# Optimization experiments

Measured on AMD Instinct MI355X. Metric: run time of the kernel, lower is better.

## Reference

```python
import jax, jax.numpy as jnp
import numpy as np

ALPHA = 3.0
TOP_K = 16
N_NODES = 8192
EMB_DIM = 128


def setup_inputs() -> dict:
    key = jax.random.key(0)
    k1, k2, k3, k4, k5, k6 = jax.random.split(key, 6)
    return {
        "idx": jnp.arange(N_NODES, dtype=jnp.int64 if jax.config.jax_enable_x64 else jnp.int32),
        "emb1_w": jax.random.normal(k1, (N_NODES, EMB_DIM), dtype=jnp.float32),
        "emb2_w": jax.random.normal(k2, (N_NODES, EMB_DIM), dtype=jnp.float32),
        "th1_w": jax.random.normal(k3, (EMB_DIM, EMB_DIM), dtype=jnp.float32) * 0.08,
        "th1_b": jax.random.normal(k4, (EMB_DIM,), dtype=jnp.float32) * 0.02,
        "th2_w": jax.random.normal(k5, (EMB_DIM, EMB_DIM), dtype=jnp.float32) * 0.08,
        "th2_b": jax.random.normal(k6, (EMB_DIM,), dtype=jnp.float32) * 0.02,
    }


def reference(idx, emb1_w, emb2_w, th1_w, th1_b, th2_w, th2_b):
    # embedding lookup + linear + tanh (nn.Linear: x @ W.T + b)
    e1 = jnp.tanh(ALPHA * (emb1_w[idx] @ th1_w.T + th1_b))  # [N, D]
    e2 = jnp.tanh(ALPHA * (emb2_w[idx] @ th2_w.T + th2_b))  # [N, D]
    # antisymmetric score -> tanh -> relu  => [N, N]
    adj = jax.nn.relu(jnp.tanh(ALPHA * (e1 @ e2.T - e2 @ e1.T)))
    # eval-mode top-k per row, scatter a binary mask (s1.fill_(1) in the source)
    _, t1 = jax.lax.top_k(adj, TOP_K)  # [N, k]
    n = idx.shape[0]
    rows = jnp.arange(n)[:, None]
    mask = jnp.zeros((n, n), dtype=adj.dtype).at[rows, t1].set(1.0)
    return adj * mask
```

## Files before the change

kernel.cpp:

```cpp
#include <hip/hip_runtime.h>

#define NN    8192
#define DD    128
#define TOPK  16

#define CUT_D 7.99881172180175781
#define CUT_F 7.99881172180175781f
#define EPS_F 2.0e-2f


__global__ __launch_bounds__(256) void k1ws(
    const int* __restrict__ idx,
    const float* __restrict__ emb1, const float* __restrict__ W1, const float* __restrict__ b1,
    const float* __restrict__ emb2, const float* __restrict__ W2, const float* __restrict__ b2,
    float* __restrict__ e1ws, float* __restrict__ e2ws)
{
    const float* emb; const float* W; const float* bias; float* eo;
    if (blockIdx.y == 0) { emb = emb1; W = W1; bias = b1; eo = e1ws; }
    else                 { emb = emb2; W = W2; bias = b2; eo = e2ws; }

    __shared__ float Wl[128][65];
    __shared__ float Xl[16][65];
    __shared__ int rowi[16];

    int t  = threadIdx.x;
    int r0 = blockIdx.x * 16;
    if (t < 16) {
        bool wide = (idx[1] == 0 && idx[2] == 1);
        int row = wide ? idx[2 * (r0 + t)] : idx[r0 + t];
        rowi[t] = min(max(row, 0), NN - 1);
    }
    __syncthreads();

    int d = t & 127, rh = t >> 7;
    double acc[8];
    #pragma unroll
    for (int q = 0; q < 8; q++) acc[q] = 0.0;

    for (int h = 0; h < 2; h++) {
        if (h) __syncthreads();
        for (int i = t; i < 128 * 64; i += 256)
            Wl[i >> 6][i & 63] = W[(i >> 6) * DD + h * 64 + (i & 63)];
        for (int i = t; i < 16 * 64; i += 256)
            Xl[i >> 6][i & 63] = emb[(size_t)rowi[i >> 6] * DD + h * 64 + (i & 63)];
        __syncthreads();
        for (int k = 0; k < 64; k++) {
            double wv = (double)Wl[d][k];
            #pragma unroll
            for (int q = 0; q < 8; q++) acc[q] += (double)Xl[rh + 2 * q][k] * wv;
        }
    }
    double bv = (double)bias[d];
    #pragma unroll
    for (int q = 0; q < 8; q++)
        eo[(size_t)(r0 + rh + 2 * q) * DD + d] = (float)tanh(3.0 * (acc[q] + bv));
}

__global__ __launch_bounds__(256) void kselfill(
    const float* __restrict__ e1, const float* __restrict__ e2,
    float* __restrict__ out)
{
    __shared__ union {
        struct { float A1[32][36], A2[32][36], B1[32][132], B2[32][132]; } p;
        float pref[32][128];
        float vals[NN];
    } sm;
    __shared__ unsigned int cls32[32][32];
    __shared__ int fb[32];
    __shared__ float redv[256];
    __shared__ int   redi[256];
    __shared__ unsigned int si[TOPK];
    __shared__ float sv[TOPK];

    int ti = blockIdx.x;
    int t  = threadIdx.x;
    int rx = t & 31, ry = t >> 5;
    int mc0 = rx * 4, mr0 = ry * 4;

    float acc[4][4];
    #pragma unroll
    for (int r = 0; r < 4; r++)
        #pragma unroll
        for (int c = 0; c < 4; c++) acc[r][c] = 0.f;

    for (int h = 0; h < 4; h++) {
        __syncthreads();
        {
            int rr = t >> 3, dq = t & 7;
            int o  = h * 32 + dq * 4;
            float4 va1 = *(const float4*)&e1[(size_t)(ti * 32 + rr) * DD + o];
            float4 va2 = *(const float4*)&e2[(size_t)(ti * 32 + rr) * DD + o];
            int dd = dq * 4;
            sm.p.A1[dd+0][rr] = va1.x; sm.p.A1[dd+1][rr] = va1.y;
            sm.p.A1[dd+2][rr] = va1.z; sm.p.A1[dd+3][rr] = va1.w;
            sm.p.A2[dd+0][rr] = va2.x; sm.p.A2[dd+1][rr] = va2.y;
            sm.p.A2[dd+2][rr] = va2.z; sm.p.A2[dd+3][rr] = va2.w;
        }
        #pragma unroll
        for (int it2 = 0; it2 < 4; it2++) {
            int id = it2 * 256 + t;
            int rr = id >> 3, dq = id & 7;
            int o  = h * 32 + dq * 4;
            float4 vb1 = *(const float4*)&e1[(size_t)rr * DD + o];
            float4 vb2 = *(const float4*)&e2[(size_t)rr * DD + o];
            int dd = dq * 4;
            sm.p.B1[dd+0][rr] = vb1.x; sm.p.B1[dd+1][rr] = vb1.y;
            sm.p.B1[dd+2][rr] = vb1.z; sm.p.B1[dd+3][rr] = vb1.w;
            sm.p.B2[dd+0][rr] = vb2.x; sm.p.B2[dd+1][rr] = vb2.y;
            sm.p.B2[dd+2][rr] = vb2.z; sm.p.B2[dd+3][rr] = vb2.w;
        }
        __syncthreads();

        #pragma unroll 4
        for (int d = 0; d < 32; d++) {
            float4 a1 = *(const float4*)&sm.p.A1[d][mr0];
            float4 a2 = *(const float4*)&sm.p.A2[d][mr0];
            float4 b1 = *(const float4*)&sm.p.B1[d][mc0];
            float4 b2 = *(const float4*)&sm.p.B2[d][mc0];
            float a1v[4] = {a1.x, a1.y, a1.z, a1.w};
            float a2v[4] = {a2.x, a2.y, a2.z, a2.w};
            float b1v[4] = {b1.x, b1.y, b1.z, b1.w};
            float b2v[4] = {b2.x, b2.y, b2.z, b2.w};
            #pragma unroll
            for (int r = 0; r < 4; r++)
                #pragma unroll
                for (int c = 0; c < 4; c++) {
                    acc[r][c] = fmaf(a1v[r],  b2v[c], acc[r][c]);
                    acc[r][c] = fmaf(-a2v[r], b1v[c], acc[r][c]);
                }
        }
    }

    #pragma unroll
    for (int r = 0; r < 4; r++) {
        unsigned int word = 0;
        #pragma unroll
        for (int c = 0; c < 4; c++) {
            float argf = 3.0f * acc[r][c];
            float del  = argf - CUT_F;
            bool sat;
            if (fabsf(del) < EPS_F) {
                int grow = ti * 32 + mr0 + r;
                int gcol = mc0 + c;
                double d1 = 0.0, d2 = 0.0;
                for (int k = 0; k < DD; k++) {
                    d1 = fma((double)e1[(size_t)grow * DD + k],
                             (double)e2[(size_t)gcol * DD + k], d1);
                    d2 = fma((double)e2[(size_t)grow * DD + k],
                             (double)e1[(size_t)gcol * DD + k], d2);
                }
                sat = (3.0 * (d1 - d2) >= CUT_D);
            } else {
                sat = (del > 0.f);
            }
            word |= (sat ? 1u : 0u) << (8 * c);
        }
        cls32[mr0 + r][rx] = word;
    }
    __syncthreads();

    {
        float4* p4 = (float4*)&sm.pref[0][0];
        #pragma unroll
        for (int i = 0; i < 4; i++) p4[i * 256 + t] = make_float4(0.f, 0.f, 0.f, 0.f);
    }
    __syncthreads();

    int wv = t >> 6, lane = t & 63;
    const unsigned char* cb = (const unsigned char*)cls32;
    for (int rr = 0; rr < 8; rr++) {
        int rloc = wv * 8 + rr;
        unsigned long long w0 = __ballot(cb[rloc * 128 + lane] != 0);
        unsigned long long w1 = __ballot(cb[rloc * 128 + 64 + lane] != 0);
        if (lane == 0) {
            if (__popcll(w0) + __popcll(w1) >= TOPK) {
                int rank = 0;
                unsigned long long x = w0; int base = 0;
                while (x && rank < TOPK) {
                    int b = __ffsll(x) - 1;
                    sm.pref[rloc][base + b] = 1.0f;
                    x &= x - 1; rank++;
                }
                x = w1; base = 64;
                while (x && rank < TOPK) {
                    int b = __ffsll(x) - 1;
                    sm.pref[rloc][base + b] = 1.0f;
                    x &= x - 1; rank++;
                }
                fb[rloc] = 0;
            } else {
                fb[rloc] = 1;
            }
        }
    }
    __syncthreads();

    for (int r = 0; r < 32; r++) {
        size_t rb = (size_t)(ti * 32 + r) * NN;
        #pragma unroll
        for (int rep = 0; rep < 2; rep++) {
            int w = rep * 256 + t;
            float4 v = (w < 32) ? *(float4*)&sm.pref[r][w * 4]
                                : make_float4(0.f, 0.f, 0.f, 0.f);
            *(float4*)&out[rb + (size_t)w * 4] = v;
        }
    }
    __syncthreads();

    for (int q = 0; q < 32; q++) {
        if (!fb[q]) continue;
        int row = ti * 32 + q;
        for (int j = t; j < NN; j += 256) {
            double d1 = 0.0, d2 = 0.0;
            for (int k = 0; k < 128; k++) {
                double r1k = (double)e1[(size_t)row * DD + k];
                double r2k = (double)e2[(size_t)row * DD + k];
                d1 = fma(r1k, (double)e2[(size_t)j * DD + k], d1);
                d2 = fma(r2k, (double)e1[(size_t)j * DD + k], d2);
            }
            double arg = 3.0 * (d1 - d2);
            float v = (arg >= CUT_D) ? 1.0f : (float)tanh(arg);
            sm.vals[j] = v > 0.f ? v : 0.f;
        }
        __syncthreads();
        for (int s = 0; s < TOPK; s++) {
            float bv = -1.f; int bj = 1 << 30;
            for (int j = t; j < NN; j += 256) {
                float v = sm.vals[j];
                if (v > bv || (v == bv && j < bj)) { bv = v; bj = j; }
            }
            redv[t] = bv; redi[t] = bj;
            __syncthreads();
            for (int sft = 128; sft > 0; sft >>= 1) {
                if (t < sft) {
                    if (redv[t + sft] > redv[t] ||
                        (redv[t + sft] == redv[t] && redi[t + sft] < redi[t])) {
                        redv[t] = redv[t + sft];
                        redi[t] = redi[t + sft];
                    }
                }
                __syncthreads();
            }
            if (t == 0) {
                si[s] = (unsigned int)redi[0];
                sv[s] = redv[0];
                sm.vals[redi[0]] = -2.f;
            }
            __syncthreads();
        }
        size_t rb = (size_t)row * NN;
        for (int w = t; w < NN / 4; w += 256) {
            float4 v = make_float4(0.f, 0.f, 0.f, 0.f);
            #pragma unroll
            for (int s = 0; s < TOPK; s++) {
                unsigned int j = si[s];
                if ((int)(j >> 2) == w) ((float*)&v)[j & 3] = sv[s];
            }
            *(float4*)&out[rb + (size_t)w * 4] = v;
        }
        __syncthreads();
    }
}

#define OFF_VAL    16
#define OFF_E1     2112
#define OFF_E2     2240

__global__ __launch_bounds__(256) void k1_fb(
    const int* __restrict__ idx,
    const float* __restrict__ emb1, const float* __restrict__ W1, const float* __restrict__ b1,
    const float* __restrict__ emb2, const float* __restrict__ W2, const float* __restrict__ b2,
    float* out)
{
    const float* emb; const float* W; const float* bias; int eoff;
    if (blockIdx.y == 0) { emb = emb1; W = W1; bias = b1; eoff = OFF_E1; }
    else                 { emb = emb2; W = W2; bias = b2; eoff = OFF_E2; }

    __shared__ float Wl[128][65];
    __shared__ float Xl[16][65];
    __shared__ int rowi[16];

    int t  = threadIdx.x;
    int r0 = blockIdx.x * 16;
    if (t < 16) {
        bool wide = (idx[1] == 0 && idx[2] == 1);
        int row = wide ? idx[2 * (r0 + t)] : idx[r0 + t];
        rowi[t] = min(max(row, 0), NN - 1);
    }
    __syncthreads();

    int d = t & 127, rh = t >> 7;
    double acc[8];
    #pragma unroll
    for (int q = 0; q < 8; q++) acc[q] = 0.0;

    for (int h = 0; h < 2; h++) {
        if (h) __syncthreads();
        for (int i = t; i < 128 * 64; i += 256)
            Wl[i >> 6][i & 63] = W[(i >> 6) * DD + h * 64 + (i & 63)];
        for (int i = t; i < 16 * 64; i += 256)
            Xl[i >> 6][i & 63] = emb[(size_t)rowi[i >> 6] * DD + h * 64 + (i & 63)];
        __syncthreads();
        for (int k = 0; k < 64; k++) {
            double wv = (double)Wl[d][k];
            #pragma unroll
            for (int q = 0; q < 8; q++) acc[q] += (double)Xl[rh + 2 * q][k] * wv;
        }
    }
    double bv = (double)bias[d];
    #pragma unroll
    for (int q = 0; q < 8; q++)
        out[(size_t)(r0 + rh + 2 * q) * NN + eoff + d] = (float)tanh(3.0 * (acc[q] + bv));
}

__global__ __launch_bounds__(256) void k2sel_fb(float* out)
{
    int ti = blockIdx.x;
    __shared__ float A1[32][68], A2[32][68], B1[32][68], B2[32][68];
    __shared__ unsigned char cls[64][128];
    __shared__ int fb[64];
    __shared__ float vals[NN];
    __shared__ float redv[256];
    __shared__ int   redi[256];

    int t  = threadIdx.x;
    int tx = t & 15, ty = t >> 4;
    int mr0 = ty * 4, mc0 = tx * 4;

    for (int tjj = 0; tjj < 2; tjj++) {
        double acc[4][4];
        #pragma unroll
        for (int r = 0; r < 4; r++)
            #pragma unroll
            for (int c = 0; c < 4; c++) acc[r][c] = 0.0;

        for (int h = 0; h < 4; h++) {
            __syncthreads();
            #pragma unroll
            for (int it2 = 0; it2 < 2; it2++) {
                int idx2 = it2 * 256 + t;
                int rr = idx2 >> 3, dq = idx2 & 7;
                int o  = h * 32 + dq * 4;
                size_t rbA = (size_t)(ti * 64 + rr) * NN;
                size_t rbB = (size_t)(tjj * 64 + rr) * NN;
                float4 v1 = *(const float4*)&out[rbA + OFF_E1 + o];
                float4 v2 = *(const float4*)&out[rbA + OFF_E2 + o];
                float4 v3 = *(const float4*)&out[rbB + OFF_E1 + o];
                float4 v4 = *(const float4*)&out[rbB + OFF_E2 + o];
                int dd = dq * 4;
                A1[dd+0][rr] = v1.x; A1[dd+1][rr] = v1.y; A1[dd+2][rr] = v1.z; A1[dd+3][rr] = v1.w;
                A2[dd+0][rr] = v2.x; A2[dd+1][rr] = v2.y; A2[dd+2][rr] = v2.z; A2[dd+3][rr] = v2.w;
                B1[dd+0][rr] = v3.x; B1[dd+1][rr] = v3.y; B1[dd+2][rr] = v3.z; B1[dd+3][rr] = v3.w;
                B2[dd+0][rr] = v4.x; B2[dd+1][rr] = v4.y; B2[dd+2][rr] = v4.z; B2[dd+3][rr] = v4.w;
            }
            __syncthreads();
            #pragma unroll 2
            for (int d = 0; d < 32; d++) {
                double a1v[4], a2v[4], b1v[4], b2v[4];
                #pragma unroll
                for (int r = 0; r < 4; r++) {
                    a1v[r] = (double)A1[d][mr0 + r];
                    a2v[r] = (double)A2[d][mr0 + r];
                }
                #pragma unroll
                for (int c = 0; c < 4; c++) {
                    b1v[c] = (double)B1[d][mc0 + c];
                    b2v[c] = (double)B2[d][mc0 + c];
                }
                #pragma unroll
                for (int r = 0; r < 4; r++)
                    #pragma unroll
                    for (int c = 0; c < 4; c++) {
                        acc[r][c] = fma(a1v[r],  b2v[c], acc[r][c]);
                        acc[r][c] = fma(-a2v[r], b1v[c], acc[r][c]);
                    }
            }
        }
        #pragma unroll
        for (int r = 0; r < 4; r++)
            #pragma unroll
            for (int c = 0; c < 4; c++)
                cls[mr0 + r][tjj * 64 + mc0 + c] = (3.0 * acc[r][c] >= CUT_D) ? 1 : 0;
    }
    __syncthreads();

    int wv = t >> 6, lane = t & 63;
    unsigned int* ou = (unsigned int*)out;
    for (int rr = 0; rr < 16; rr++) {
        int rloc = wv * 16 + rr;
        unsigned long long w0 = __ballot(cls[rloc][lane] != 0);
        unsigned long long w1 = __ballot(cls[rloc][64 + lane] != 0);
        if (lane == 0) {
            size_t rb = (size_t)(ti * 64 + rloc) * NN;
            if (__popcll(w0) + __popcll(w1) >= TOPK) {
                int rank = 0;
                unsigned long long x = w0; int base = 0;
                while (x && rank < TOPK) {
                    int b = __ffsll(x) - 1;
                    ou[rb + rank] = (unsigned int)(base + b);
                    out[rb + OFF_VAL + rank] = 1.0f;
                    x &= x - 1; rank++;
                }
                x = w1; base = 64;
                while (x && rank < TOPK) {
                    int b = __ffsll(x) - 1;
                    ou[rb + rank] = (unsigned int)(base + b);
                    out[rb + OFF_VAL + rank] = 1.0f;
                    x &= x - 1; rank++;
                }
                fb[rloc] = 0;
            } else fb[rloc] = 1;
        }
    }
    __syncthreads();

    for (int q = 0; q < 64; q++) {
        if (!fb[q]) continue;
        int row = ti * 64 + q;
        size_t rb = (size_t)row * NN;
        const float* r1 = &out[rb + OFF_E1];
        const float* r2 = &out[rb + OFF_E2];
        for (int j = t; j < NN; j += 256) {
            const float* e1j = &out[(size_t)j * NN + OFF_E1];
            const float* e2j = &out[(size_t)j * NN + OFF_E2];
            double d1 = 0.0, d2 = 0.0;
            for (int k = 0; k < 128; k++) {
                d1 = fma((double)r1[k], (double)e2j[k], d1);
                d2 = fma((double)r2[k], (double)e1j[k], d2);
            }
            double arg = 3.0 * (d1 - d2);
            float v = (arg >= CUT_D) ? 1.0f : (float)tanh(arg);
            vals[j] = v > 0.f ? v : 0.f;
        }
        __syncthreads();
        for (int s = 0; s < TOPK; s++) {
            float bv = -1.f; int bj = 1 << 30;
            for (int j = t; j < NN; j += 256) {
                float v = vals[j];
                if (v > bv || (v == bv && j < bj)) { bv = v; bj = j; }
            }
            redv[t] = bv; redi[t] = bj;
            __syncthreads();
            for (int sft = 128; sft > 0; sft >>= 1) {
                if (t < sft) {
                    if (redv[t + sft] > redv[t] ||
                        (redv[t + sft] == redv[t] && redi[t + sft] < redi[t])) {
                        redv[t] = redv[t + sft];
                        redi[t] = redi[t + sft];
                    }
                }
                __syncthreads();
            }
            if (t == 0) {
                ou[rb + s]            = (unsigned int)redi[0];
                out[rb + OFF_VAL + s] = redv[0];
                vals[redi[0]] = -2.f;
            }
            __syncthreads();
        }
        __syncthreads();
    }
}

__global__ __launch_bounds__(256) void k5_fb(float* out)
{
    __shared__ unsigned int si[TOPK];
    __shared__ float sv[TOPK];
    int t = threadIdx.x;
    size_t rb = (size_t)blockIdx.x * NN;
    if (t < TOPK) {
        si[t] = ((const unsigned int*)out)[rb + t];
        sv[t] = out[rb + OFF_VAL + t];
    }
    __syncthreads();

    unsigned int li[TOPK]; float lv[TOPK];
    #pragma unroll
    for (int s = 0; s < TOPK; s++) { li[s] = si[s]; lv[s] = sv[s]; }

    #pragma unroll
    for (int it2 = 0; it2 < 8; it2++) {
        unsigned int w = it2 * 256 + t;
        float4 v = make_float4(0.f, 0.f, 0.f, 0.f);
        #pragma unroll
        for (int s = 0; s < TOPK; s++) {
            unsigned int j = li[s];
            if ((j >> 2) == w) ((float*)&v)[j & 3] = lv[s];
        }
        *(float4*)&out[rb + (size_t)w * 4] = v;
    }
}

extern "C" void kernel_launch(void* const* d_in, const int* in_sizes, int n_in,
                              void* d_out, int out_size, void* d_ws, size_t ws_size,
                              hipStream_t stream)
{
    (void)in_sizes; (void)n_in; (void)out_size;

    const int*   idx  = (const int*)  d_in[0];
    const float* emb1 = (const float*)d_in[1];
    const float* emb2 = (const float*)d_in[2];
    const float* th1w = (const float*)d_in[3];
    const float* th1b = (const float*)d_in[4];
    const float* th2w = (const float*)d_in[5];
    const float* th2b = (const float*)d_in[6];
    float* out = (float*)d_out;

    const size_t need = 2ull * NN * DD * sizeof(float);
    if (d_ws != nullptr && ws_size >= need) {
        float* e1ws = (float*)d_ws;
        float* e2ws = e1ws + (size_t)NN * DD;
        k1ws    <<<dim3(NN / 16, 2), 256, 0, stream>>>(idx, emb1, th1w, th1b,
                                                       emb2, th2w, th2b, e1ws, e2ws);
        kselfill<<<NN / 32,          256, 0, stream>>>(e1ws, e2ws, out);
    } else {
        k1_fb   <<<dim3(NN / 16, 2), 256, 0, stream>>>(idx, emb1, th1w, th1b,
                                                       emb2, th2w, th2b, out);
        k2sel_fb<<<NN / 64,          256, 0, stream>>>(out);
        k5_fb   <<<NN,               256, 0, stream>>>(out);
    }
}
```

Before: 117.8 us.

## Halve rows per block and compact near-threshold entries into a suspect list

Each select-and-fill block now handles 16 rows instead of 32, so the grid doubles to 512 blocks and spreads better across the GPU's compute units. Per-thread accumulators shrink from 4x4 to 2x4. Entries whose score sits near the saturation cutoff are now queued in a shared suspect list and recomputed in double precision by all threads together, instead of inside each thread's own divergent loop. If the list overflows, the affected rows fall back to the full exact path, which adds an atomic counter and some extra synchronisation.

Measured after the change: 104.1 us. 1.13x faster.

```diff
diff --git a/kernel.cpp b/kernel.cpp
--- a/kernel.cpp
+++ b/kernel.cpp
@@ -3,10 +3,12 @@
 #define NN    8192
 #define DD    128
 #define TOPK  16
+#define RPB   16
 
 #define CUT_D 7.99881172180175781
 #define CUT_F 7.99881172180175781f
 #define EPS_F 2.0e-2f
+#define MAXSUS 512
 
 
 __global__ __launch_bounds__(256) void k1ws(
@@ -61,12 +63,14 @@
     float* __restrict__ out)
 {
     __shared__ union {
-        struct { float A1[32][36], A2[32][36], B1[32][132], B2[32][132]; } p;
-        float pref[32][128];
+        struct { float A1[32][20], A2[32][20], B1[32][132], B2[32][132]; } p;
+        float pref[RPB][128];
         float vals[NN];
     } sm;
-    __shared__ unsigned int cls32[32][32];
-    __shared__ int fb[32];
+    __shared__ unsigned char cls[RPB][128];
+    __shared__ unsigned int suspects[MAXSUS];
+    __shared__ unsigned int nsus;
+    __shared__ int fb[RPB];
     __shared__ float redv[256];
     __shared__ int   redi[256];
     __shared__ unsigned int si[TOPK];
@@ -75,21 +79,23 @@
     int ti = blockIdx.x;
     int t  = threadIdx.x;
     int rx = t & 31, ry = t >> 5;
-    int mc0 = rx * 4, mr0 = ry * 4;
-
-    float acc[4][4];
-    #pragma unroll
-    for (int r = 0; r < 4; r++)
+    int mc0 = rx * 4, mr0 = ry * 2;
+
+    if (t == 0) nsus = 0;
+
+    float acc[2][4];
+    #pragma unroll
+    for (int r = 0; r < 2; r++)
         #pragma unroll
         for (int c = 0; c < 4; c++) acc[r][c] = 0.f;
 
     for (int h = 0; h < 4; h++) {
         __syncthreads();
-        {
+        if (t < 128) {
             int rr = t >> 3, dq = t & 7;
             int o  = h * 32 + dq * 4;
-            float4 va1 = *(const float4*)&e1[(size_t)(ti * 32 + rr) * DD + o];
-            float4 va2 = *(const float4*)&e2[(size_t)(ti * 32 + rr) * DD + o];
+            float4 va1 = *(const float4*)&e1[(size_t)(ti * RPB + rr) * DD + o];
+            float4 va2 = *(const float4*)&e2[(size_t)(ti * RPB + rr) * DD + o];
             int dd = dq * 4;
             sm.p.A1[dd+0][rr] = va1.x; sm.p.A1[dd+1][rr] = va1.y;
             sm.p.A1[dd+2][rr] = va1.z; sm.p.A1[dd+3][rr] = va1.w;
@@ -113,16 +119,18 @@
 
         #pragma unroll 4
         for (int d = 0; d < 32; d++) {
-            float4 a1 = *(const float4*)&sm.p.A1[d][mr0];
-            float4 a2 = *(const float4*)&sm.p.A2[d][mr0];
+            float a1v[2], a2v[2];
+            #pragma unroll
+            for (int r = 0; r < 2; r++) {
+                a1v[r] = sm.p.A1[d][mr0 + r];
+                a2v[r] = sm.p.A2[d][mr0 + r];
+            }
             float4 b1 = *(const float4*)&sm.p.B1[d][mc0];
             float4 b2 = *(const float4*)&sm.p.B2[d][mc0];
-            float a1v[4] = {a1.x, a1.y, a1.z, a1.w};
-            float a2v[4] = {a2.x, a2.y, a2.z, a2.w};
             float b1v[4] = {b1.x, b1.y, b1.z, b1.w};
             float b2v[4] = {b2.x, b2.y, b2.z, b2.w};
             #pragma unroll
-            for (int r = 0; r < 4; r++)
+            for (int r = 0; r < 2; r++)
                 #pragma unroll
                 for (int c = 0; c < 4; c++) {
                     acc[r][c] = fmaf(a1v[r],  b2v[c], acc[r][c]);
@@ -132,46 +140,47 @@
     }
 
     #pragma unroll
-    for (int r = 0; r < 4; r++) {
-        unsigned int word = 0;
+    for (int r = 0; r < 2; r++)
         #pragma unroll
         for (int c = 0; c < 4; c++) {
-            float argf = 3.0f * acc[r][c];
-            float del  = argf - CUT_F;
-            bool sat;
+            float del = 3.0f * acc[r][c] - CUT_F;
+            cls[mr0 + r][mc0 + c] = (del > 0.f) ? 1 : 0;
             if (fabsf(del) < EPS_F) {
-                int grow = ti * 32 + mr0 + r;
-                int gcol = mc0 + c;
-                double d1 = 0.0, d2 = 0.0;
-                for (int k = 0; k < DD; k++) {
-                    d1 = fma((double)e1[(size_t)grow * DD + k],
-                             (double)e2[(size_t)gcol * DD + k], d1);
-                    d2 = fma((double)e2[(size_t)grow * DD + k],
-                             (double)e1[(size_t)gcol * DD + k], d2);
-                }
-                sat = (3.0 * (d1 - d2) >= CUT_D);
-            } else {
-                sat = (del > 0.f);
-            }
-            word |= (sat ? 1u : 0u) << (8 * c);
-        }
-        cls32[mr0 + r][rx] = word;
+                unsigned int slot = atomicAdd(&nsus, 1u);
+                if (slot < MAXSUS)
+                    suspects[slot] = ((unsigned int)(mr0 + r) << 8) | (unsigned int)(mc0 + c);
+            }
+        }
+    __syncthreads();
+
+    {
+        unsigned int n = nsus < MAXSUS ? nsus : MAXSUS;
+        for (unsigned int s = t; s < n; s += 256) {
+            int r = (int)(suspects[s] >> 8), c = (int)(suspects[s] & 255u);
+            size_t grow = (size_t)(ti * RPB + r) * DD;
+            size_t gcol = (size_t)c * DD;
+            double d1 = 0.0, d2 = 0.0;
+            for (int k = 0; k < DD; k++) {
+                d1 = fma((double)e1[grow + k], (double)e2[gcol + k], d1);
+                d2 = fma((double)e2[grow + k], (double)e1[gcol + k], d2);
+            }
+            cls[r][c] = (3.0 * (d1 - d2) >= CUT_D) ? 1 : 0;
+        }
     }
     __syncthreads();
 
     {
         float4* p4 = (float4*)&sm.pref[0][0];
         #pragma unroll
-        for (int i = 0; i < 4; i++) p4[i * 256 + t] = make_float4(0.f, 0.f, 0.f, 0.f);
+        for (int i = 0; i < 2; i++) p4[i * 256 + t] = make_float4(0.f, 0.f, 0.f, 0.f);
     }
     __syncthreads();
 
     int wv = t >> 6, lane = t & 63;
-    const unsigned char* cb = (const unsigned char*)cls32;
-    for (int rr = 0; rr < 8; rr++) {
-        int rloc = wv * 8 + rr;
-        unsigned long long w0 = __ballot(cb[rloc * 128 + lane] != 0);
-        unsigned long long w1 = __ballot(cb[rloc * 128 + 64 + lane] != 0);
+    for (int rr = 0; rr < 4; rr++) {
+        int rloc = wv * 4 + rr;
+        unsigned long long w0 = __ballot(cls[rloc][lane] != 0);
+        unsigned long long w1 = __ballot(cls[rloc][64 + lane] != 0);
         if (lane == 0) {
             if (__popcll(w0) + __popcll(w1) >= TOPK) {
                 int rank = 0;
@@ -193,10 +202,11 @@
             }
         }
     }
-    __syncthreads();
-
-    for (int r = 0; r < 32; r++) {
-        size_t rb = (size_t)(ti * 32 + r) * NN;
+    if (t < RPB && nsus > MAXSUS) fb[t] = 1;
+    __syncthreads();
+
+    for (int r = 0; r < RPB; r++) {
+        size_t rb = (size_t)(ti * RPB + r) * NN;
         #pragma unroll
         for (int rep = 0; rep < 2; rep++) {
             int w = rep * 256 + t;
@@ -207,9 +217,9 @@
     }
     __syncthreads();
 
-    for (int q = 0; q < 32; q++) {
+    for (int q = 0; q < RPB; q++) {
         if (!fb[q]) continue;
-        int row = ti * 32 + q;
+        int row = ti * RPB + q;
         for (int j = t; j < NN; j += 256) {
             double d1 = 0.0, d2 = 0.0;
             for (int k = 0; k < 128; k++) {
@@ -512,7 +522,7 @@
         float* e2ws = e1ws + (size_t)NN * DD;
         k1ws    <<<dim3(NN / 16, 2), 256, 0, stream>>>(idx, emb1, th1w, th1b,
                                                        emb2, th2w, th2b, e1ws, e2ws);
-        kselfill<<<NN / 32,          256, 0, stream>>>(e1ws, e2ws, out);
+        kselfill<<<NN / RPB,         256, 0, stream>>>(e1ws, e2ws, out);
     } else {
         k1_fb   <<<dim3(NN / 16, 2), 256, 0, stream>>>(idx, emb1, th1w, th1b,
                                                        emb2, th2w, th2b, out);
```

## Zero output with memset, scatter top-k entries and batch borderline rechecks

Applied to the files above, without the earlier changes.

The selection kernel no longer streams zeros over every output row. The host now issues hipMemsetAsync over the whole output before the kernels, and the kernel scatters only the top-k values, using single-element writes for the fast path and for fallback rows. Borderline cells near the saturation cutoff are gathered into a shared suspect list and rechecked in double precision by all threads in parallel, instead of inside each thread's own accumulator loop. This adds a separate memset pass and an atomic counter in shared memory; if the suspect list overflows, the whole tile takes the slow fallback path.

New measurement: 119.2 us. About the same (+1.2%).

```diff
diff --git a/kernel.cpp b/kernel.cpp
--- a/kernel.cpp
+++ b/kernel.cpp
@@ -7,6 +7,7 @@
 #define CUT_D 7.99881172180175781
 #define CUT_F 7.99881172180175781f
 #define EPS_F 2.0e-2f
+#define MAXSUS 512
 
 
 __global__ __launch_bounds__(256) void k1ws(
@@ -56,17 +57,20 @@
         eo[(size_t)(r0 + rh + 2 * q) * DD + d] = (float)tanh(3.0 * (acc[q] + bv));
 }
 
-__global__ __launch_bounds__(256) void kselfill(
+__global__ __launch_bounds__(256) void ksel32(
     const float* __restrict__ e1, const float* __restrict__ e2,
     float* __restrict__ out)
 {
     __shared__ union {
         struct { float A1[32][36], A2[32][36], B1[32][132], B2[32][132]; } p;
-        float pref[32][128];
         float vals[NN];
     } sm;
-    __shared__ unsigned int cls32[32][32];
+    __shared__ unsigned char cls[32][128];
+    __shared__ int idxs[32][TOPK];
+    __shared__ unsigned int suspects[MAXSUS];
+    __shared__ unsigned int nsus;
     __shared__ int fb[32];
+    __shared__ int anyfb;
     __shared__ float redv[256];
     __shared__ int   redi[256];
     __shared__ unsigned int si[TOPK];
@@ -76,6 +80,8 @@
     int t  = threadIdx.x;
     int rx = t & 31, ry = t >> 5;
     int mc0 = rx * 4, mr0 = ry * 4;
+
+    if (t == 0) { nsus = 0; anyfb = 0; }
 
     float acc[4][4];
     #pragma unroll
@@ -132,79 +138,76 @@
     }
 
     #pragma unroll
-    for (int r = 0; r < 4; r++) {
-        unsigned int word = 0;
+    for (int r = 0; r < 4; r++)
         #pragma unroll
         for (int c = 0; c < 4; c++) {
-            float argf = 3.0f * acc[r][c];
-            float del  = argf - CUT_F;
-            bool sat;
+            float del = 3.0f * acc[r][c] - CUT_F;
+            cls[mr0 + r][mc0 + c] = (del > 0.f) ? 1 : 0;
             if (fabsf(del) < EPS_F) {
-                int grow = ti * 32 + mr0 + r;
-                int gcol = mc0 + c;
-                double d1 = 0.0, d2 = 0.0;
-                for (int k = 0; k < DD; k++) {
-                    d1 = fma((double)e1[(size_t)grow * DD + k],
-                             (double)e2[(size_t)gcol * DD + k], d1);
-                    d2 = fma((double)e2[(size_t)grow * DD + k],
-                             (double)e1[(size_t)gcol * DD + k], d2);
-                }
-                sat = (3.0 * (d1 - d2) >= CUT_D);
-            } else {
-                sat = (del > 0.f);
-            }
-            word |= (sat ? 1u : 0u) << (8 * c);
-        }
-        cls32[mr0 + r][rx] = word;
-    }
+                unsigned int slot = atomicAdd(&nsus, 1u);
+                if (slot < MAXSUS)
+                    suspects[slot] = ((unsigned int)(mr0 + r) << 8) | (unsigned int)(mc0 + c);
+            }
+        }
     __syncthreads();
 
     {
-        float4* p4 = (float4*)&sm.pref[0][0];
-        #pragma unroll
-        for (int i = 0; i < 4; i++) p4[i * 256 + t] = make_float4(0.f, 0.f, 0.f, 0.f);
-    }
+        unsigned int n = nsus < MAXSUS ? nsus : MAXSUS;
+        for (unsigned int s = t; s < n; s += 256) {
+            int r = (int)(suspects[s] >> 8), c = (int)(suspects[s] & 255u);
+            size_t grow = (size_t)(ti * 32 + r) * DD;
+            size_t gcol = (size_t)c * DD;
+            double d1 = 0.0, d2 = 0.0;
+            for (int k = 0; k < DD; k++) {
+                d1 = fma((double)e1[grow + k], (double)e2[gcol + k], d1);
+                d2 = fma((double)e2[grow + k], (double)e1[gcol + k], d2);
+            }
+            cls[r][c] = (3.0 * (d1 - d2) >= CUT_D) ? 1 : 0;
+        }
+    }
+    for (int i = t; i < 32 * TOPK; i += 256) idxs[i >> 4][i & 15] = -1;
     __syncthreads();
 
     int wv = t >> 6, lane = t & 63;
-    const unsigned char* cb = (const unsigned char*)cls32;
     for (int rr = 0; rr < 8; rr++) {
         int rloc = wv * 8 + rr;
-        unsigned long long w0 = __ballot(cb[rloc * 128 + lane] != 0);
-        unsigned long long w1 = __ballot(cb[rloc * 128 + 64 + lane] != 0);
+        unsigned long long w0 = __ballot(cls[rloc][lane] != 0);
+        unsigned long long w1 = __ballot(cls[rloc][64 + lane] != 0);
         if (lane == 0) {
-            if (__popcll(w0) + __popcll(w1) >= TOPK) {
+            bool ok = (__popcll(w0) + __popcll(w1) >= TOPK) &&
+                      !(nsus > MAXSUS);
+            if (ok) {
                 int rank = 0;
                 unsigned long long x = w0; int base = 0;
                 while (x && rank < TOPK) {
                     int b = __ffsll(x) - 1;
-                    sm.pref[rloc][base + b] = 1.0f;
+                    idxs[rloc][rank] = base + b;
                     x &= x - 1; rank++;
                 }
                 x = w1; base = 64;
                 while (x && rank < TOPK) {
                     int b = __ffsll(x) - 1;
-                    sm.pref[rloc][base + b] = 1.0f;
+                    idxs[rloc][rank] = base + b;
                     x &= x - 1; rank++;
                 }
                 fb[rloc] = 0;
             } else {
                 fb[rloc] = 1;
-            }
-        }
-    }
-    __syncthreads();
-
-    for (int r = 0; r < 32; r++) {
-        size_t rb = (size_t)(ti * 32 + r) * NN;
-        #pragma unroll
-        for (int rep = 0; rep < 2; rep++) {
-            int w = rep * 256 + t;
-            float4 v = (w < 32) ? *(float4*)&sm.pref[r][w * 4]
-                                : make_float4(0.f, 0.f, 0.f, 0.f);
-            *(float4*)&out[rb + (size_t)w * 4] = v;
-        }
-    }
+                anyfb = 1;
+                #pragma unroll
+                for (int s = 0; s < TOPK; s++) idxs[rloc][s] = -1;
+            }
+        }
+    }
+    __syncthreads();
+
+    for (int i = t; i < 32 * TOPK; i += 256) {
+        int r = i >> 4, col = idxs[r][i & 15];
+        if (col >= 0)
+            out[(size_t)(ti * 32 + r) * NN + col] = 1.0f;
+    }
+
+    if (!anyfb) return;
     __syncthreads();
 
     for (int q = 0; q < 32; q++) {
@@ -248,16 +251,8 @@
             }
             __syncthreads();
         }
-        size_t rb = (size_t)row * NN;
-        for (int w = t; w < NN / 4; w += 256) {
-            float4 v = make_float4(0.f, 0.f, 0.f, 0.f);
-            #pragma unroll
-            for (int s = 0; s < TOPK; s++) {
-                unsigned int j = si[s];
-                if ((int)(j >> 2) == w) ((float*)&v)[j & 3] = sv[s];
-            }
-            *(float4*)&out[rb + (size_t)w * 4] = v;
-        }
+        if (t < TOPK)
+            out[(size_t)row * NN + si[t]] = sv[t];
         __syncthreads();
     }
 }
@@ -510,9 +505,10 @@
     if (d_ws != nullptr && ws_size >= need) {
         float* e1ws = (float*)d_ws;
         float* e2ws = e1ws + (size_t)NN * DD;
-        k1ws    <<<dim3(NN / 16, 2), 256, 0, stream>>>(idx, emb1, th1w, th1b,
-                                                       emb2, th2w, th2b, e1ws, e2ws);
-        kselfill<<<NN / 32,          256, 0, stream>>>(e1ws, e2ws, out);
+        hipMemsetAsync(out, 0, (size_t)NN * NN * sizeof(float), stream);
+        k1ws  <<<dim3(NN / 16, 2), 256, 0, stream>>>(idx, emb1, th1w, th1b,
+                                                     emb2, th2w, th2b, e1ws, e2ws);
+        ksel32<<<NN / 32,          256, 0, stream>>>(e1ws, e2ws, out);
     } else {
         k1_fb   <<<dim3(NN / 16, 2), 256, 0, stream>>>(idx, emb1, th1w, th1b,
                                                        emb2, th2w, th2b, out);
```
